# Performance work log

Measured on AMD Instinct MI355X. Metric: run time of the kernel, lower is better.

Reference implementation:

```python
import jax, jax.numpy as jnp
import numpy as np

D_MODEL = 1024
D_INNER = 2 * D_MODEL          # expand=2
D_STATE = 16
D_CONV = 4
DT_RANK = D_MODEL // 16        # ceil(1024/16)
BATCH, SEQ = 4, 1024
LN_EPS = 1e-5
LRELU_SLOPE = 0.01


def setup_inputs() -> dict:
    key = jax.random.key(0)
    ks = jax.random.split(key, 12)
    s = 0.02
    return {
        "x": jax.random.normal(ks[0], (BATCH, SEQ, D_MODEL), jnp.float32),
        "W_in": jax.random.normal(ks[1], (D_MODEL, 2 * D_INNER), jnp.float32) * s,
        "conv_w": jax.random.normal(ks[2], (D_INNER, D_CONV), jnp.float32) * s,
        "conv_b": jnp.zeros((D_INNER,), jnp.float32),
        "W_x": jax.random.normal(ks[3], (D_INNER, DT_RANK + 2 * D_STATE), jnp.float32) * s,
        "W_dt": jax.random.normal(ks[4], (DT_RANK, D_INNER), jnp.float32) * s,
        "b_dt": jax.random.normal(ks[5], (D_INNER,), jnp.float32) * 0.1 - 4.0,
        "A_log": jnp.log(jnp.broadcast_to(jnp.arange(1, D_STATE + 1, dtype=jnp.float32), (D_INNER, D_STATE))),
        "D": jnp.ones((D_INNER,), jnp.float32),
        "W_out": jax.random.normal(ks[6], (D_INNER, D_MODEL), jnp.float32) * s,
        "gamma": jnp.ones((D_MODEL,), jnp.float32),
        "beta": jnp.zeros((D_MODEL,), jnp.float32),
    }


def _selective_scan(u, dt, A, B, C, Dp):
    # u, dt: (b, l, d); A: (d, n); B, C: (b, l, n); Dp: (d,)
    dA = jnp.exp(dt[..., None] * A)                       # (b, l, d, n)
    dBu = dt[..., None] * B[:, :, None, :] * u[..., None]  # (b, l, d, n)

    def step(h, inp):
        dA_t, dBu_t, C_t = inp                            # (b,d,n),(b,d,n),(b,n)
        h = dA_t * h + dBu_t
        y = jnp.einsum("bdn,bn->bd", h, C_t)
        return h, y

    h0 = jnp.zeros((u.shape[0], u.shape[2], A.shape[1]), u.dtype)
    xs = (dA.transpose(1, 0, 2, 3), dBu.transpose(1, 0, 2, 3), C.transpose(1, 0, 2))
    _, ys = jax.lax.scan(step, h0, xs)                    # ys: (l, b, d)
    return ys.transpose(1, 0, 2) + u * Dp                 # (b, l, d)


def _mamba(x, W_in, conv_w, conv_b, W_x, W_dt, b_dt, A_log, Dp, W_out):
    xz = x @ W_in                                          # (b, l, 2*di)
    xc, z = jnp.split(xz, 2, axis=-1)
    # causal depthwise conv over time
    xc_t = xc.transpose(0, 2, 1)                           # (b, di, l)
    kern = conv_w[:, None, :]                              # (di, 1, k)
    conv = jax.lax.conv_general_dilated(
        xc_t, kern, window_strides=(1,), padding=[(D_CONV - 1, 0)],
        dimension_numbers=("NCH", "OIH", "NCH"), feature_group_count=D_INNER)
    xc = jax.nn.silu(conv + conv_b[None, :, None]).transpose(0, 2, 1)  # (b, l, di)

    x_dbl = xc @ W_x                                       # (b, l, dt_rank + 2n)
    dt, Bm, Cm = jnp.split(x_dbl, [DT_RANK, DT_RANK + D_STATE], axis=-1)
    dt = jax.nn.softplus(dt @ W_dt + b_dt)                 # (b, l, di)
    A = -jnp.exp(A_log)                                    # (di, n)

    y = _selective_scan(xc, dt, A, Bm, Cm, Dp)             # (b, l, di)
    y = y * jax.nn.silu(z)
    return y @ W_out                                       # (b, l, d_model)


def reference(x, W_in, conv_w, conv_b, W_x, W_dt, b_dt, A_log, D, W_out, gamma, beta):
    h = x + _mamba(x, W_in, conv_w, conv_b, W_x, W_dt, b_dt, A_log, D, W_out)
    mu = jnp.mean(h, axis=-1, keepdims=True)
    var = jnp.mean(jnp.square(h - mu), axis=-1, keepdims=True)
    h = (h - mu) * jax.lax.rsqrt(var + LN_EPS) * gamma + beta
    return jnp.where(h >= 0, h, LRELU_SLOPE * h)
```

## Files before the change

### kernel.cpp

```cpp
#include <hip/hip_runtime.h>
#include <hip/hip_fp16.h>
#include <cstdint>
#include <cstddef>

typedef _Float16 f16x8 __attribute__((ext_vector_type(8)));
typedef _Float16 f16x4 __attribute__((ext_vector_type(4)));
typedef float    f32x4 __attribute__((ext_vector_type(4)));

#define TC  32
#define NCH 32

__device__ __forceinline__ float sigmoidf_(float x) { return 1.f / (1.f + __expf(-x)); }

__device__ __forceinline__ void gload_lds16(const _Float16* g, _Float16* l) {
  __builtin_amdgcn_global_load_lds(
      (const __attribute__((address_space(1))) void*)g,
      (__attribute__((address_space(3))) void*)l, 16, 0, 0);
}

__global__ __launch_bounds__(256) void k_cast16(const float* __restrict__ src,
                                                _Float16* __restrict__ dst, int n4) {
  int i = blockIdx.x * 256 + threadIdx.x;
  if (i < n4) {
    float4 v = ((const float4*)src)[i];
    f16x4 o = {(_Float16)v.x, (_Float16)v.y, (_Float16)v.z, (_Float16)v.w};
    ((f16x4*)dst)[i] = o;
  }
}

__global__ void k_transpose16(const float* __restrict__ src, _Float16* __restrict__ dst,
                              int R, int C, int Cpad) {
  __shared__ float tile[32][33];
  int c0 = blockIdx.x * 32, r0 = blockIdx.y * 32;
  int tx = threadIdx.x, ty = threadIdx.y;
  #pragma unroll
  for (int i = 0; i < 32; i += 8) {
    int r = r0 + ty + i, c = c0 + tx;
    tile[ty + i][tx] = (r < R && c < C) ? src[(size_t)r * C + c] : 0.f;
  }
  __syncthreads();
  #pragma unroll
  for (int i = 0; i < 32; i += 8) {
    int cc = c0 + ty + i, rr = r0 + tx;
    if (cc < Cpad && rr < R) dst[(size_t)cc * R + rr] = (_Float16)tile[tx][ty + i];
  }
}

template <int EPI>
__global__ __launch_bounds__(256) void k_gemm_bt(
    const _Float16* __restrict__ A,
    const _Float16* __restrict__ BT,
    float* __restrict__ C,
    _Float16* __restrict__ C16,
    _Float16* __restrict__ AUX,
    const float* __restrict__ bias,
    int M, int N, int K)
{
  __shared__ __align__(16) _Float16 As[128 * 64];
  __shared__ __align__(16) _Float16 Bs[128 * 64];
  const int tid  = threadIdx.x;
  const int lane = tid & 63;
  const int wave = tid >> 6;
  const int wm = (wave >> 1) * 64;
  const int wn = (wave & 1) * 64;
  const int l15 = lane & 15;
  const int q   = lane >> 4;
  const int m0 = blockIdx.y * 128;
  const int n0 = blockIdx.x * 128;

  const int kpb = K / gridDim.z;
  const int k0  = blockIdx.z * kpb;

  const int rch = lane >> 3;
  const int g   = (lane & 7) ^ (rch & 7);
  const _Float16* gA = A  + (size_t)(m0 + wave * 32 + rch) * K + k0 + g * 8;
  const _Float16* gB = BT + (size_t)(n0 + wave * 32 + rch) * K + k0 + g * 8;
  _Float16* lA = As + wave * 32 * 64 + lane * 8;
  _Float16* lB = Bs + wave * 32 * 64 + lane * 8;

  const int sx = l15 & 7;

  f32x4 acc[4][4] = {};

  for (int k = 0; k < kpb; k += 64) {
    #pragma unroll
    for (int c = 0; c < 4; ++c) {
      gload_lds16(gA + (size_t)(c * 8) * K + k, lA + c * 512);
      gload_lds16(gB + (size_t)(c * 8) * K + k, lB + c * 512);
    }
    __syncthreads();
    #pragma unroll
    for (int k32 = 0; k32 < 2; ++k32) {
      f16x8 af[4], bf[4];
      #pragma unroll
      for (int i = 0; i < 4; ++i) {
        af[i] = *(const f16x8*)&As[(wm + i * 16 + l15) * 64 + ((k32 * 4 + q) ^ sx) * 8];
        bf[i] = *(const f16x8*)&Bs[(wn + i * 16 + l15) * 64 + ((k32 * 4 + q) ^ sx) * 8];
      }
      #pragma unroll
      for (int mi = 0; mi < 4; ++mi)
        #pragma unroll
        for (int ni = 0; ni < 4; ++ni)
          acc[mi][ni] = __builtin_amdgcn_mfma_f32_16x16x32_f16(af[mi], bf[ni], acc[mi][ni], 0, 0, 0);
    }
    __syncthreads();
  }

  #pragma unroll
  for (int mi = 0; mi < 4; ++mi) {
    #pragma unroll
    for (int ni = 0; ni < 4; ++ni) {
      int col = n0 + wn + ni * 16 + l15;
      #pragma unroll
      for (int r = 0; r < 4; ++r) {
        int row = m0 + wm + mi * 16 + q * 4 + r;
        float v = acc[mi][ni][r];
        if constexpr (EPI == 2) {
          float t = v + bias[col];
          float sp = (t > 20.f) ? t : log1pf(__expf(t));
          AUX[(size_t)row * N + col] = (_Float16)sp;
        } else if constexpr (EPI == 3) {
          if (col < 2048) {
            C16[(size_t)row * 2048 + col] = (_Float16)v;
          } else {
            AUX[(size_t)row * 2048 + (col - 2048)] = (_Float16)(v * sigmoidf_(v));
          }
        } else {
          C[(size_t)blockIdx.z * M * N + (size_t)row * N + col] = v;
        }
      }
    }
  }
}

__global__ __launch_bounds__(256) void k_red4(const float* __restrict__ Cp,
                                              float* __restrict__ xdbl,
                                              _Float16* __restrict__ dtin) {
  int i = blockIdx.x * 256 + threadIdx.x;
  const int PL = 4096 * 128;
  float s = Cp[i] + Cp[i + PL] + Cp[i + 2 * PL] + Cp[i + 3 * PL];
  xdbl[i] = s;
  int col = i & 127;
  if (col < 64) dtin[(size_t)(i >> 7) * 64 + col] = (_Float16)s;
}

__global__ __launch_bounds__(256) void k_conv_silu(
    const _Float16* __restrict__ xc, const float* __restrict__ cw,
    const float* __restrict__ cb, _Float16* __restrict__ out)
{
  int idx = blockIdx.x * 256 + threadIdx.x;
  int d = idx & 2047;
  int row = idx >> 11;
  int t = row & 1023;
  const _Float16* p = xc + (size_t)row * 2048 + d;
  float acc = cb[d] + cw[d * 4 + 3] * (float)p[0];
  if (t >= 1) acc += cw[d * 4 + 2] * (float)p[-2048];
  if (t >= 2) acc += cw[d * 4 + 1] * (float)p[-4096];
  if (t >= 3) acc += cw[d * 4 + 0] * (float)p[-6144];
  out[idx] = (_Float16)(acc * sigmoidf_(acc));
}

__global__ __launch_bounds__(256) void k_scan_part(
    const _Float16* __restrict__ dt, const _Float16* __restrict__ u,
    const float* __restrict__ xdbl, const float* __restrict__ A_log,
    float* __restrict__ P, float* __restrict__ S)
{
  const int tid = threadIdx.x;
  const int d = blockIdx.x * 256 + tid;
  const int c = blockIdx.y;
  const int b = blockIdx.z;
  const int row0 = b * 1024 + c * TC;
  __shared__ float Bs[TC * 16];
  for (int i = tid; i < TC * 16; i += 256) {
    int t = i >> 4, n = i & 15;
    Bs[i] = xdbl[(size_t)(row0 + t) * 128 + 64 + n];
  }
  float a[16];
  #pragma unroll
  for (int n = 0; n < 16; ++n) a[n] = -__expf(A_log[d * 16 + n]);
  float h[16] = {};
  float sumdt = 0.f;
  __syncthreads();
  for (int t = 0; t < TC; ++t) {
    const int row = row0 + t;
    float dtv = (float)dt[(size_t)row * 2048 + d];
    float uv  = (float)u[(size_t)row * 2048 + d];
    float dtu = dtv * uv;
    sumdt += dtv;
    #pragma unroll
    for (int n = 0; n < 16; ++n)
      h[n] = h[n] * __expf(dtv * a[n]) + dtu * Bs[t * 16 + n];
  }
  const size_t base = (size_t)(b * NCH + c) * 16 * 2048 + d;
  #pragma unroll
  for (int n = 0; n < 16; ++n) {
    P[base + n * 2048] = __expf(sumdt * a[n]);
    S[base + n * 2048] = h[n];
  }
}

__global__ __launch_bounds__(256) void k_scan_comb(
    float* __restrict__ P, const float* __restrict__ S)
{
  int idx = blockIdx.x * 256 + threadIdx.x;
  int d = idx & 2047;
  int n = (idx >> 11) & 15;
  int b = idx >> 15;
  float H = 0.f;
  for (int c = 0; c < NCH - 1; ++c) {
    size_t off = ((size_t)(b * NCH + c) * 16 + n) * 2048 + d;
    H = P[off] * H + S[off];
    P[off] = H;
  }
}

__global__ __launch_bounds__(256) void k_scan_y(
    const _Float16* __restrict__ dt, const _Float16* __restrict__ u,
    const _Float16* __restrict__ zs, const float* __restrict__ xdbl,
    const float* __restrict__ A_log, const float* __restrict__ Hbuf,
    const float* __restrict__ Dv, _Float16* __restrict__ ys)
{
  const int tid = threadIdx.x;
  const int d = blockIdx.x * 256 + tid;
  const int c = blockIdx.y;
  const int b = blockIdx.z;
  const int row0 = b * 1024 + c * TC;
  __shared__ float Bs[TC * 16];
  __shared__ float Cs[TC * 16];
  for (int i = tid; i < TC * 16; i += 256) {
    int t = i >> 4, n = i & 15;
    Bs[i] = xdbl[(size_t)(row0 + t) * 128 + 64 + n];
    Cs[i] = xdbl[(size_t)(row0 + t) * 128 + 80 + n];
  }
  float a[16];
  #pragma unroll
  for (int n = 0; n < 16; ++n) a[n] = -__expf(A_log[d * 16 + n]);
  float h[16];
  if (c == 0) {
    #pragma unroll
    for (int n = 0; n < 16; ++n) h[n] = 0.f;
  } else {
    const size_t hb = (size_t)(b * NCH + (c - 1)) * 16 * 2048 + d;
    #pragma unroll
    for (int n = 0; n < 16; ++n) h[n] = Hbuf[hb + n * 2048];
  }
  const float Dd = Dv[d];
  __syncthreads();
  for (int t = 0; t < TC; ++t) {
    const int row = row0 + t;
    float dtv = (float)dt[(size_t)row * 2048 + d];
    float uv  = (float)u[(size_t)row * 2048 + d];
    float zv  = (float)zs[(size_t)row * 2048 + d];
    float dtu = dtv * uv;
    float y = uv * Dd;
    #pragma unroll
    for (int n = 0; n < 16; ++n) {
      h[n] = h[n] * __expf(dtv * a[n]) + dtu * Bs[t * 16 + n];
      y = fmaf(h[n], Cs[t * 16 + n], y);
    }
    ys[(size_t)row * 2048 + d] = (_Float16)(y * zv);
  }
}

__global__ __launch_bounds__(256) void k_resid_ln(
    const float* __restrict__ x, const float* __restrict__ yp,
    const float* __restrict__ gamma, const float* __restrict__ beta,
    float* __restrict__ out)
{
  int row = blockIdx.x;
  int tid = threadIdx.x;
  const int PL = 4096 * 1024;
  float v[4];
  float s = 0.f, s2 = 0.f;
  #pragma unroll
  for (int i = 0; i < 4; ++i) {
    int c = tid + i * 256;
    size_t off = (size_t)row * 1024 + c;
    float h = x[off] + yp[off] + yp[off + PL];
    v[i] = h; s += h; s2 += h * h;
  }
  #pragma unroll
  for (int off = 32; off > 0; off >>= 1) {
    s  += __shfl_down(s, off, 64);
    s2 += __shfl_down(s2, off, 64);
  }
  __shared__ float rs[4], rs2[4];
  int wv = tid >> 6, ln = tid & 63;
  if (ln == 0) { rs[wv] = s; rs2[wv] = s2; }
  __syncthreads();
  if (tid == 0) {
    float a = 0.f, b2 = 0.f;
    #pragma unroll
    for (int i = 0; i < 4; ++i) { a += rs[i]; b2 += rs2[i]; }
    rs[0] = a; rs2[0] = b2;
  }
  __syncthreads();
  float mu  = rs[0] * (1.f / 1024.f);
  float var = rs2[0] * (1.f / 1024.f) - mu * mu;
  float inv = rsqrtf(var + 1e-5f);
  #pragma unroll
  for (int i = 0; i < 4; ++i) {
    int c = tid + i * 256;
    float hn = (v[i] - mu) * inv * gamma[c] + beta[c];
    out[(size_t)row * 1024 + c] = hn >= 0.f ? hn : 0.01f * hn;
  }
}

extern "C" void kernel_launch(void* const* d_in, const int* in_sizes, int n_in,
                              void* d_out, int out_size, void* d_ws, size_t ws_size,
                              hipStream_t stream)
{
  const float* x     = (const float*)d_in[0];
  const float* W_in  = (const float*)d_in[1];
  const float* convw = (const float*)d_in[2];
  const float* convb = (const float*)d_in[3];
  const float* W_x   = (const float*)d_in[4];
  const float* W_dt  = (const float*)d_in[5];
  const float* b_dt  = (const float*)d_in[6];
  const float* A_log = (const float*)d_in[7];
  const float* Dv    = (const float*)d_in[8];
  const float* W_out = (const float*)d_in[9];
  const float* gamma = (const float*)d_in[10];
  const float* beta  = (const float*)d_in[11];
  float* out = (float*)d_out;

  char* ws = (char*)d_ws;
  const size_t MB = 1ull << 20;
  _Float16* x16   = (_Float16*)(ws + 0 * MB);
  _Float16* WinT  = (_Float16*)(ws + 8 * MB);
  _Float16* xc16  = (_Float16*)(ws + 16 * MB);
  _Float16* zsil  = (_Float16*)(ws + 32 * MB);
  _Float16* xcs   = (_Float16*)(ws + 48 * MB);
  _Float16* dtb   = (_Float16*)(ws + 64 * MB);
  _Float16* WxT   = (_Float16*)(ws + 80 * MB);
  float*    xdbl  = (float*)   (ws + 80 * MB + 512 * 1024);
  _Float16* dtin  = (_Float16*)(ws + 82 * MB + 512 * 1024);
  _Float16* WdtT  = (_Float16*)(ws + 83 * MB);
  _Float16* WoutT = (_Float16*)(ws + 84 * MB);
  _Float16* ysb   = (_Float16*)(ws + 88 * MB);
  float*    Cpart = (float*)   (ws + 16 * MB);
  float*    Pb    = (float*)   (ws + 16 * MB);
  float*    Sb    = (float*)   (ws + 0 * MB);
  float*    yp    = (float*)   (ws + 0 * MB);

  k_cast16<<<4096 * 1024 / 4 / 256, 256, 0, stream>>>(x, x16, 4096 * 1024 / 4);
  k_transpose16<<<dim3(4096 / 32, 1024 / 32), dim3(32, 8), 0, stream>>>(W_in, WinT, 1024, 4096, 4096);
  k_gemm_bt<3><<<dim3(32, 32), 256, 0, stream>>>(x16, WinT, nullptr, xc16, zsil, nullptr, 4096, 4096, 1024);
  k_conv_silu<<<4096 * 2048 / 256, 256, 0, stream>>>(xc16, convw, convb, xcs);
  k_transpose16<<<dim3(128 / 32, 2048 / 32), dim3(32, 8), 0, stream>>>(W_x, WxT, 2048, 96, 128);
  k_gemm_bt<4><<<dim3(1, 32, 4), 256, 0, stream>>>(xcs, WxT, Cpart, nullptr, nullptr, nullptr, 4096, 128, 2048);
  k_red4<<<4096 * 128 / 256, 256, 0, stream>>>(Cpart, xdbl, dtin);
  k_transpose16<<<dim3(2048 / 32, 64 / 32), dim3(32, 8), 0, stream>>>(W_dt, WdtT, 64, 2048, 2048);
  k_gemm_bt<2><<<dim3(16, 32), 256, 0, stream>>>(dtin, WdtT, nullptr, nullptr, dtb, b_dt, 4096, 2048, 64);
  k_scan_part<<<dim3(8, NCH, 4), 256, 0, stream>>>(dtb, xcs, xdbl, A_log, Pb, Sb);
  k_scan_comb<<<4 * 16 * 2048 / 256, 256, 0, stream>>>(Pb, Sb);
  k_scan_y<<<dim3(8, NCH, 4), 256, 0, stream>>>(dtb, xcs, zsil, xdbl, A_log, Pb, Dv, ysb);
  k_transpose16<<<dim3(1024 / 32, 2048 / 32), dim3(32, 8), 0, stream>>>(W_out, WoutT, 2048, 1024, 1024);
  k_gemm_bt<4><<<dim3(8, 32, 2), 256, 0, stream>>>(ysb, WoutT, yp, nullptr, nullptr, nullptr, 4096, 1024, 2048);
  k_resid_ln<<<4096, 256, 0, stream>>>(x, yp, gamma, beta, out);
}
```

Measured before the change: 386.5 us.

## Fuse prep transposes, partial-sum reduction, and scan phases into fewer kernels

Merges the input cast and the four weight transposes into one `k_prep` launch. Folds the split-K partial reduction into the dt-projection GEMM, which sums the four partials while staging its A tile. Replaces the three scan kernels with one cooperative kernel that uses grid-wide syncs between the chunk-local pass, the cross-chunk combine and the output pass. This removes several launches and the intermediate xdbl/dtin buffers. In exchange the scan runs with half as many threads, each looping over two channel halves, adds two grid barriers, and `ys` is written in place over the `dt` buffer.

```diff
diff --git a/kernel.cpp b/kernel.cpp
--- a/kernel.cpp
+++ b/kernel.cpp
@@ -1,7 +1,10 @@
 #include <hip/hip_runtime.h>
 #include <hip/hip_fp16.h>
+#include <hip/hip_cooperative_groups.h>
 #include <cstdint>
 #include <cstddef>
+
+namespace cg = cooperative_groups;
 
 typedef _Float16 f16x8 __attribute__((ext_vector_type(8)));
 typedef _Float16 f16x4 __attribute__((ext_vector_type(4)));
@@ -18,31 +21,49 @@
       (__attribute__((address_space(3))) void*)l, 16, 0, 0);
 }
 
-__global__ __launch_bounds__(256) void k_cast16(const float* __restrict__ src,
-                                                _Float16* __restrict__ dst, int n4) {
-  int i = blockIdx.x * 256 + threadIdx.x;
-  if (i < n4) {
-    float4 v = ((const float4*)src)[i];
+__device__ __forceinline__ void t16_body(const float* __restrict__ src,
+    _Float16* __restrict__ dst, int R, int C, int Cpad, int bx, int by,
+    int tid, float tile[32][33]) {
+  int c0 = bx * 32, r0 = by * 32, tx = tid & 31, ty = tid >> 5;
+  #pragma unroll
+  for (int i = 0; i < 4; ++i) {
+    int r = r0 + ty + i * 8, c = c0 + tx;
+    tile[ty + i * 8][tx] = (r < R && c < C) ? src[(size_t)r * C + c] : 0.f;
+  }
+  __syncthreads();
+  #pragma unroll
+  for (int i = 0; i < 4; ++i) {
+    int cc = c0 + ty + i * 8, rr = r0 + tx;
+    if (cc < Cpad && rr < R) dst[(size_t)cc * R + rr] = (_Float16)tile[tx][ty + i * 8];
+  }
+}
+
+__global__ __launch_bounds__(256) void k_prep(
+    const float* __restrict__ x, _Float16* __restrict__ x16,
+    const float* __restrict__ W_in, _Float16* __restrict__ WinT,
+    const float* __restrict__ W_x, _Float16* __restrict__ WxT,
+    const float* __restrict__ W_dt, _Float16* __restrict__ WdtT,
+    const float* __restrict__ W_out, _Float16* __restrict__ WoutT)
+{
+  __shared__ float tile[32][33];
+  const int blk = blockIdx.x, tid = threadIdx.x;
+  if (blk < 4096) {
+    int i = blk * 256 + tid;
+    float4 v = ((const float4*)x)[i];
     f16x4 o = {(_Float16)v.x, (_Float16)v.y, (_Float16)v.z, (_Float16)v.w};
-    ((f16x4*)dst)[i] = o;
-  }
-}
-
-__global__ void k_transpose16(const float* __restrict__ src, _Float16* __restrict__ dst,
-                              int R, int C, int Cpad) {
-  __shared__ float tile[32][33];
-  int c0 = blockIdx.x * 32, r0 = blockIdx.y * 32;
-  int tx = threadIdx.x, ty = threadIdx.y;
-  #pragma unroll
-  for (int i = 0; i < 32; i += 8) {
-    int r = r0 + ty + i, c = c0 + tx;
-    tile[ty + i][tx] = (r < R && c < C) ? src[(size_t)r * C + c] : 0.f;
-  }
-  __syncthreads();
-  #pragma unroll
-  for (int i = 0; i < 32; i += 8) {
-    int cc = c0 + ty + i, rr = r0 + tx;
-    if (cc < Cpad && rr < R) dst[(size_t)cc * R + rr] = (_Float16)tile[tx][ty + i];
+    ((f16x4*)x16)[i] = o;
+  } else if (blk < 8192) {
+    int b = blk - 4096;
+    t16_body(W_in, WinT, 1024, 4096, 4096, b & 127, b >> 7, tid, tile);
+  } else if (blk < 8448) {
+    int b = blk - 8192;
+    t16_body(W_x, WxT, 2048, 96, 128, b & 3, b >> 2, tid, tile);
+  } else if (blk < 8576) {
+    int b = blk - 8448;
+    t16_body(W_dt, WdtT, 64, 2048, 2048, b & 63, b >> 6, tid, tile);
+  } else {
+    int b = blk - 8576;
+    t16_body(W_out, WoutT, 2048, 1024, 1024, b & 31, b >> 5, tid, tile);
   }
 }
 
@@ -53,7 +74,6 @@
     float* __restrict__ C,
     _Float16* __restrict__ C16,
     _Float16* __restrict__ AUX,
-    const float* __restrict__ bias,
     int M, int N, int K)
 {
   __shared__ __align__(16) _Float16 As[128 * 64];
@@ -115,11 +135,7 @@
       for (int r = 0; r < 4; ++r) {
         int row = m0 + wm + mi * 16 + q * 4 + r;
         float v = acc[mi][ni][r];
-        if constexpr (EPI == 2) {
-          float t = v + bias[col];
-          float sp = (t > 20.f) ? t : log1pf(__expf(t));
-          AUX[(size_t)row * N + col] = (_Float16)sp;
-        } else if constexpr (EPI == 3) {
+        if constexpr (EPI == 3) {
           if (col < 2048) {
             C16[(size_t)row * 2048 + col] = (_Float16)v;
           } else {
@@ -133,15 +149,76 @@
   }
 }
 
-__global__ __launch_bounds__(256) void k_red4(const float* __restrict__ Cp,
-                                              float* __restrict__ xdbl,
-                                              _Float16* __restrict__ dtin) {
-  int i = blockIdx.x * 256 + threadIdx.x;
+__global__ __launch_bounds__(256) void k_g3(
+    const float* __restrict__ Cpart,
+    const _Float16* __restrict__ BT,
+    const float* __restrict__ bias,
+    _Float16* __restrict__ AUX)
+{
+  __shared__ __align__(16) _Float16 As2[128 * 72];
+  __shared__ __align__(16) _Float16 Bs[128 * 64];
+  const int tid  = threadIdx.x;
+  const int lane = tid & 63;
+  const int wave = tid >> 6;
+  const int wm = (wave >> 1) * 64;
+  const int wn = (wave & 1) * 64;
+  const int l15 = lane & 15;
+  const int q   = lane >> 4;
+  const int m0 = blockIdx.y * 128;
+  const int n0 = blockIdx.x * 128;
   const int PL = 4096 * 128;
-  float s = Cp[i] + Cp[i + PL] + Cp[i + 2 * PL] + Cp[i + 3 * PL];
-  xdbl[i] = s;
-  int col = i & 127;
-  if (col < 64) dtin[(size_t)(i >> 7) * 64 + col] = (_Float16)s;
+
+  #pragma unroll
+  for (int i = 0; i < 4; ++i) {
+    int idx = i * 256 + tid;
+    int r = idx >> 3, s = idx & 7;
+    const float* p = Cpart + (size_t)(m0 + r) * 128 + s * 8;
+    f16x8 o;
+    #pragma unroll
+    for (int j = 0; j < 8; ++j)
+      o[j] = (_Float16)(p[j] + p[j + PL] + p[j + 2 * PL] + p[j + 3 * PL]);
+    *(f16x8*)&As2[r * 72 + s * 8] = o;
+  }
+  const int rch = lane >> 3;
+  const int g   = (lane & 7) ^ (rch & 7);
+  const _Float16* gB = BT + (size_t)(n0 + wave * 32 + rch) * 64 + g * 8;
+  _Float16* lB = Bs + wave * 32 * 64 + lane * 8;
+  #pragma unroll
+  for (int c = 0; c < 4; ++c)
+    gload_lds16(gB + (size_t)(c * 8) * 64, lB + c * 512);
+  __syncthreads();
+
+  const int sx = l15 & 7;
+  f32x4 acc[4][4] = {};
+  #pragma unroll
+  for (int k32 = 0; k32 < 2; ++k32) {
+    f16x8 af[4], bf[4];
+    #pragma unroll
+    for (int i = 0; i < 4; ++i) {
+      af[i] = *(const f16x8*)&As2[(wm + i * 16 + l15) * 72 + (k32 * 4 + q) * 8];
+      bf[i] = *(const f16x8*)&Bs[(wn + i * 16 + l15) * 64 + ((k32 * 4 + q) ^ sx) * 8];
+    }
+    #pragma unroll
+    for (int mi = 0; mi < 4; ++mi)
+      #pragma unroll
+      for (int ni = 0; ni < 4; ++ni)
+        acc[mi][ni] = __builtin_amdgcn_mfma_f32_16x16x32_f16(af[mi], bf[ni], acc[mi][ni], 0, 0, 0);
+  }
+
+  #pragma unroll
+  for (int mi = 0; mi < 4; ++mi) {
+    #pragma unroll
+    for (int ni = 0; ni < 4; ++ni) {
+      int col = n0 + wn + ni * 16 + l15;
+      #pragma unroll
+      for (int r = 0; r < 4; ++r) {
+        int row = m0 + wm + mi * 16 + q * 4 + r;
+        float t = acc[mi][ni][r] + bias[col];
+        float sp = (t > 20.f) ? t : log1pf(__expf(t));
+        AUX[(size_t)row * 2048 + col] = (_Float16)sp;
+      }
+    }
+  }
 }
 
 __global__ __launch_bounds__(256) void k_conv_silu(
@@ -160,105 +237,97 @@
   out[idx] = (_Float16)(acc * sigmoidf_(acc));
 }
 
-__global__ __launch_bounds__(256) void k_scan_part(
+__global__ __launch_bounds__(256, 2) void k_scan_all(
     const _Float16* __restrict__ dt, const _Float16* __restrict__ u,
-    const float* __restrict__ xdbl, const float* __restrict__ A_log,
-    float* __restrict__ P, float* __restrict__ S)
-{
+    const _Float16* __restrict__ zs, const float* __restrict__ Cpart,
+    const float* __restrict__ A_log, const float* __restrict__ Dv,
+    float* __restrict__ P, float* __restrict__ S, _Float16* __restrict__ ys)
+{
+  cg::grid_group gg = cg::this_grid();
   const int tid = threadIdx.x;
-  const int d = blockIdx.x * 256 + tid;
-  const int c = blockIdx.y;
-  const int b = blockIdx.z;
+  const int blk = blockIdx.x;
+  const int xb = blk & 3;
+  const int c  = (blk >> 2) & 31;
+  const int b  = blk >> 7;
   const int row0 = b * 1024 + c * TC;
-  __shared__ float Bs[TC * 16];
+  const int PL = 4096 * 128;
+  __shared__ float Bs[TC * 16], Cs[TC * 16];
   for (int i = tid; i < TC * 16; i += 256) {
     int t = i >> 4, n = i & 15;
-    Bs[i] = xdbl[(size_t)(row0 + t) * 128 + 64 + n];
-  }
-  float a[16];
-  #pragma unroll
-  for (int n = 0; n < 16; ++n) a[n] = -__expf(A_log[d * 16 + n]);
-  float h[16] = {};
-  float sumdt = 0.f;
+    const float* p = Cpart + (size_t)(row0 + t) * 128 + 64 + n;
+    Bs[i] = p[0] + p[PL] + p[2 * PL] + p[3 * PL];
+    Cs[i] = p[16] + p[16 + PL] + p[16 + 2 * PL] + p[16 + 3 * PL];
+  }
   __syncthreads();
-  for (int t = 0; t < TC; ++t) {
-    const int row = row0 + t;
-    float dtv = (float)dt[(size_t)row * 2048 + d];
-    float uv  = (float)u[(size_t)row * 2048 + d];
-    float dtu = dtv * uv;
-    sumdt += dtv;
-    #pragma unroll
-    for (int n = 0; n < 16; ++n)
-      h[n] = h[n] * __expf(dtv * a[n]) + dtu * Bs[t * 16 + n];
-  }
-  const size_t base = (size_t)(b * NCH + c) * 16 * 2048 + d;
-  #pragma unroll
-  for (int n = 0; n < 16; ++n) {
-    P[base + n * 2048] = __expf(sumdt * a[n]);
-    S[base + n * 2048] = h[n];
-  }
-}
-
-__global__ __launch_bounds__(256) void k_scan_comb(
-    float* __restrict__ P, const float* __restrict__ S)
-{
-  int idx = blockIdx.x * 256 + threadIdx.x;
-  int d = idx & 2047;
-  int n = (idx >> 11) & 15;
-  int b = idx >> 15;
-  float H = 0.f;
-  for (int c = 0; c < NCH - 1; ++c) {
-    size_t off = ((size_t)(b * NCH + c) * 16 + n) * 2048 + d;
-    H = P[off] * H + S[off];
-    P[off] = H;
-  }
-}
-
-__global__ __launch_bounds__(256) void k_scan_y(
-    const _Float16* __restrict__ dt, const _Float16* __restrict__ u,
-    const _Float16* __restrict__ zs, const float* __restrict__ xdbl,
-    const float* __restrict__ A_log, const float* __restrict__ Hbuf,
-    const float* __restrict__ Dv, _Float16* __restrict__ ys)
-{
-  const int tid = threadIdx.x;
-  const int d = blockIdx.x * 256 + tid;
-  const int c = blockIdx.y;
-  const int b = blockIdx.z;
-  const int row0 = b * 1024 + c * TC;
-  __shared__ float Bs[TC * 16];
-  __shared__ float Cs[TC * 16];
-  for (int i = tid; i < TC * 16; i += 256) {
-    int t = i >> 4, n = i & 15;
-    Bs[i] = xdbl[(size_t)(row0 + t) * 128 + 64 + n];
-    Cs[i] = xdbl[(size_t)(row0 + t) * 128 + 80 + n];
-  }
-  float a[16];
-  #pragma unroll
-  for (int n = 0; n < 16; ++n) a[n] = -__expf(A_log[d * 16 + n]);
-  float h[16];
-  if (c == 0) {
-    #pragma unroll
-    for (int n = 0; n < 16; ++n) h[n] = 0.f;
-  } else {
-    const size_t hb = (size_t)(b * NCH + (c - 1)) * 16 * 2048 + d;
-    #pragma unroll
-    for (int n = 0; n < 16; ++n) h[n] = Hbuf[hb + n * 2048];
-  }
-  const float Dd = Dv[d];
-  __syncthreads();
-  for (int t = 0; t < TC; ++t) {
-    const int row = row0 + t;
-    float dtv = (float)dt[(size_t)row * 2048 + d];
-    float uv  = (float)u[(size_t)row * 2048 + d];
-    float zv  = (float)zs[(size_t)row * 2048 + d];
-    float dtu = dtv * uv;
-    float y = uv * Dd;
+  #pragma unroll 1
+  for (int half = 0; half < 2; ++half) {
+    const int d = xb * 512 + half * 256 + tid;
+    float a[16];
+    #pragma unroll
+    for (int n = 0; n < 16; ++n) a[n] = -__expf(A_log[d * 16 + n]);
+    float h[16] = {};
+    float sumdt = 0.f;
+    for (int t = 0; t < TC; ++t) {
+      const int row = row0 + t;
+      float dtv = (float)dt[(size_t)row * 2048 + d];
+      float uv  = (float)u[(size_t)row * 2048 + d];
+      float dtu = dtv * uv;
+      sumdt += dtv;
+      #pragma unroll
+      for (int n = 0; n < 16; ++n)
+        h[n] = h[n] * __expf(dtv * a[n]) + dtu * Bs[t * 16 + n];
+    }
+    const size_t base = (size_t)(b * NCH + c) * 16 * 2048 + d;
     #pragma unroll
     for (int n = 0; n < 16; ++n) {
-      h[n] = h[n] * __expf(dtv * a[n]) + dtu * Bs[t * 16 + n];
-      y = fmaf(h[n], Cs[t * 16 + n], y);
-    }
-    ys[(size_t)row * 2048 + d] = (_Float16)(y * zv);
+      P[base + n * 2048] = __expf(sumdt * a[n]);
+      S[base + n * 2048] = h[n];
+    }
+  }
+  __threadfence();
+  gg.sync();
+  {
+    int idx = blk * 256 + tid;
+    int dd = idx & 2047, nn = (idx >> 11) & 15, bb = idx >> 15;
+    float H = 0.f;
+    for (int cc = 0; cc < NCH - 1; ++cc) {
+      size_t off = ((size_t)(bb * NCH + cc) * 16 + nn) * 2048 + dd;
+      H = P[off] * H + S[off];
+      P[off] = H;
+    }
+  }
+  __threadfence();
+  gg.sync();
+  #pragma unroll 1
+  for (int half = 0; half < 2; ++half) {
+    const int d = xb * 512 + half * 256 + tid;
+    float a[16];
+    #pragma unroll
+    for (int n = 0; n < 16; ++n) a[n] = -__expf(A_log[d * 16 + n]);
+    float h[16];
+    if (c == 0) {
+      #pragma unroll
+      for (int n = 0; n < 16; ++n) h[n] = 0.f;
+    } else {
+      const size_t hb = (size_t)(b * NCH + (c - 1)) * 16 * 2048 + d;
+      #pragma unroll
+      for (int n = 0; n < 16; ++n) h[n] = P[hb + n * 2048];
+    }
+    const float Dd = Dv[d];
+    for (int t = 0; t < TC; ++t) {
+      const int row = row0 + t;
+      float dtv = (float)dt[(size_t)row * 2048 + d];
+      float uv  = (float)u[(size_t)row * 2048 + d];
+      float zv  = (float)zs[(size_t)row * 2048 + d];
+      float dtu = dtv * uv;
+      float y = uv * Dd;
+      #pragma unroll
+      for (int n = 0; n < 16; ++n) {
+        h[n] = h[n] * __expf(dtv * a[n]) + dtu * Bs[t * 16 + n];
+        y = fmaf(h[n], Cs[t * 16 + n], y);
+      }
+      ys[(size_t)row * 2048 + d] = (_Float16)(y * zv);
+    }
   }
 }
 
@@ -333,29 +402,26 @@
   _Float16* xcs   = (_Float16*)(ws + 48 * MB);
   _Float16* dtb   = (_Float16*)(ws + 64 * MB);
   _Float16* WxT   = (_Float16*)(ws + 80 * MB);
-  float*    xdbl  = (float*)   (ws + 80 * MB + 512 * 1024);
-  _Float16* dtin  = (_Float16*)(ws + 82 * MB + 512 * 1024);
-  _Float16* WdtT  = (_Float16*)(ws + 83 * MB);
-  _Float16* WoutT = (_Float16*)(ws + 84 * MB);
-  _Float16* ysb   = (_Float16*)(ws + 88 * MB);
-  float*    Cpart = (float*)   (ws + 16 * MB);
-  float*    Pb    = (float*)   (ws + 16 * MB);
-  float*    Sb    = (float*)   (ws + 0 * MB);
+  _Float16* WdtT  = (_Float16*)(ws + 80 * MB + 512 * 1024);
+  _Float16* WoutT = (_Float16*)(ws + 81 * MB);
+  float*    Cpart = (float*)   (ws + 85 * MB);
+  float*    Pb    = (float*)   (ws + 0 * MB);
+  float*    Sb    = (float*)   (ws + 16 * MB);
+  _Float16* ysb   = dtb;
   float*    yp    = (float*)   (ws + 0 * MB);
 
-  k_cast16<<<4096 * 1024 / 4 / 256, 256, 0, stream>>>(x, x16, 4096 * 1024 / 4);
-  k_transpose16<<<dim3(4096 / 32, 1024 / 32), dim3(32, 8), 0, stream>>>(W_in, WinT, 1024, 4096, 4096);
-  k_gemm_bt<3><<<dim3(32, 32), 256, 0, stream>>>(x16, WinT, nullptr, xc16, zsil, nullptr, 4096, 4096, 1024);
+  k_prep<<<10624, 256, 0, stream>>>(x, x16, W_in, WinT, W_x, WxT, W_dt, WdtT, W_out, WoutT);
+  k_gemm_bt<3><<<dim3(32, 32), 256, 0, stream>>>(x16, WinT, nullptr, xc16, zsil, 4096, 4096, 1024);
   k_conv_silu<<<4096 * 2048 / 256, 256, 0, stream>>>(xc16, convw, convb, xcs);
-  k_transpose16<<<dim3(128 / 32, 2048 / 32), dim3(32, 8), 0, stream>>>(W_x, WxT, 2048, 96, 128);
-  k_gemm_bt<4><<<dim3(1, 32, 4), 256, 0, stream>>>(xcs, WxT, Cpart, nullptr, nullptr, nullptr, 4096, 128, 2048);
-  k_red4<<<4096 * 128 / 256, 256, 0, stream>>>(Cpart, xdbl, dtin);
-  k_transpose16<<<dim3(2048 / 32, 64 / 32), dim3(32, 8), 0, stream>>>(W_dt, WdtT, 64, 2048, 2048);
-  k_gemm_bt<2><<<dim3(16, 32), 256, 0, stream>>>(dtin, WdtT, nullptr, nullptr, dtb, b_dt, 4096, 2048, 64);
-  k_scan_part<<<dim3(8, NCH, 4), 256, 0, stream>>>(dtb, xcs, xdbl, A_log, Pb, Sb);
-  k_scan_comb<<<4 * 16 * 2048 / 256, 256, 0, stream>>>(Pb, Sb);
-  k_scan_y<<<dim3(8, NCH, 4), 256, 0, stream>>>(dtb, xcs, zsil, xdbl, A_log, Pb, Dv, ysb);
-  k_transpose16<<<dim3(1024 / 32, 2048 / 32), dim3(32, 8), 0, stream>>>(W_out, WoutT, 2048, 1024, 1024);
-  k_gemm_bt<4><<<dim3(8, 32, 2), 256, 0, stream>>>(ysb, WoutT, yp, nullptr, nullptr, nullptr, 4096, 1024, 2048);
+  k_gemm_bt<4><<<dim3(1, 32, 4), 256, 0, stream>>>(xcs, WxT, Cpart, nullptr, nullptr, 4096, 128, 2048);
+  k_g3<<<dim3(16, 32), 256, 0, stream>>>(Cpart, WdtT, b_dt, dtb);
+  {
+    const _Float16* a0 = dtb; const _Float16* a1 = xcs; const _Float16* a2 = zsil;
+    const float* a3 = Cpart; const float* a4 = A_log; const float* a5 = Dv;
+    float* a6 = Pb; float* a7 = Sb; _Float16* a8 = ysb;
+    void* args[] = {&a0, &a1, &a2, &a3, &a4, &a5, &a6, &a7, &a8};
+    hipLaunchCooperativeKernel((void*)k_scan_all, dim3(512), dim3(256), args, 0, stream);
+  }
+  k_gemm_bt<4><<<dim3(8, 32, 2), 256, 0, stream>>>(ysb, WoutT, yp, nullptr, nullptr, 4096, 1024, 2048);
   k_resid_ln<<<4096, 256, 0, stream>>>(x, yp, gamma, beta, out);
 }
```

Result: slower. 645.4 us (+67.0%).
